# Optimization experiments

Measured on AMD Instinct MI355X. Metric: run time of the kernel, lower is better.

## Reference

```python
import jax, jax.numpy as jnp
import numpy as np

HIDDEN = 1024
NUM_CLASSES = 10
NUM_GAUSSIANS = 8
IN_FEATURES = 16
HEADS = NUM_CLASSES * NUM_GAUSSIANS * IN_FEATURES * 2  # 2560 tiny Linear(hidden,1) heads


def setup_inputs() -> dict:
    key = jax.random.key(0)
    kx, kw, kb = jax.random.split(key, 3)
    x = jax.random.normal(kx, (8192, HIDDEN), dtype=jnp.float32)
    # Stacked weights of the 2560 per-head Linear(hidden,1) layers.
    bound = 1.0 / np.sqrt(HIDDEN)
    W = jax.random.uniform(kw, (HIDDEN, HEADS), minval=-bound, maxval=bound, dtype=jnp.float32)
    b = jax.random.uniform(kb, (HEADS,), minval=-bound, maxval=bound, dtype=jnp.float32)
    return {"x": x, "W": W, "b": b}


def reference(x, W, b):
    batch = x.shape[0]
    # Fused form of the Python loop of Linear(hidden,1)+Sigmoid per head.
    z = jax.nn.sigmoid(x @ W + b)  # [batch, HEADS]
    return z.reshape(batch, NUM_CLASSES, NUM_GAUSSIANS, IN_FEATURES, 2)
```

## Files before the change

kernel.cpp:

```cpp
#include <hip/hip_runtime.h>
#include <hip/hip_bf16.h>

#define HIDDEN 1024
#define HEADS  2560

#define BM 256
#define BN 320
#define BK 64
#define NT (HIDDEN / BK)
#define AREG 0
#define ABYTES (BM * BK * 2)
#define BBYTES (BN * BK * 2)
#define BUFSZ  (ABYTES + BBYTES)

typedef float  f32x4  __attribute__((ext_vector_type(4)));
typedef __bf16 bf16x8 __attribute__((ext_vector_type(8)));
typedef __bf16 bf16x4 __attribute__((ext_vector_type(4)));

__device__ __forceinline__ void gload_lds16(const void* g, void* l) {
    __builtin_amdgcn_global_load_lds(
        (const __attribute__((address_space(1))) unsigned int*)g,
        (__attribute__((address_space(3))) unsigned int*)l, 16, 0, 0);
}
__device__ __forceinline__ unsigned swz(unsigned x) {
    return x ^ (((x >> 7) & 7u) << 4);
}

__global__ __launch_bounds__(256)
void cvt_x(const float* __restrict__ x, __bf16* __restrict__ xc, int n8)
{
    int idx = blockIdx.x * blockDim.x + threadIdx.x;
    int stride = gridDim.x * blockDim.x;
    for (int i = idx; i < n8; i += stride) {
        const float4 a = *reinterpret_cast<const float4*>(x + (size_t)i * 8);
        const float4 b = *reinterpret_cast<const float4*>(x + (size_t)i * 8 + 4);
        bf16x8 h;
        h[0] = (__bf16)a.x; h[1] = (__bf16)a.y; h[2] = (__bf16)a.z; h[3] = (__bf16)a.w;
        h[4] = (__bf16)b.x; h[5] = (__bf16)b.y; h[6] = (__bf16)b.z; h[7] = (__bf16)b.w;
        *reinterpret_cast<bf16x8*>(xc + (size_t)i * 8) = h;
    }
}

__global__ __launch_bounds__(256)
void cvt_w(const float* __restrict__ W, __bf16* __restrict__ Wt)
{
    __shared__ __bf16 tile[64][72];
    const int t  = threadIdx.x;
    const int n0 = blockIdx.x * 64;
    const int k0 = blockIdx.y * 64;

    #pragma unroll
    for (int i = 0; i < 4; ++i) {
        const int k    = (t >> 4) + i * 16;
        const int col4 = (t & 15) * 4;
        const float4 v = *reinterpret_cast<const float4*>(
            W + (size_t)(k0 + k) * HEADS + n0 + col4);
        bf16x4 h;
        h[0] = (__bf16)v.x; h[1] = (__bf16)v.y; h[2] = (__bf16)v.z; h[3] = (__bf16)v.w;
        *reinterpret_cast<bf16x4*>(&tile[k][col4]) = h;
    }
    __syncthreads();
    #pragma unroll
    for (int i = 0; i < 4; ++i) {
        const int n  = (t >> 4) + i * 16;
        const int k4 = (t & 15) * 4;
        bf16x4 h;
        h[0] = tile[k4 + 0][n]; h[1] = tile[k4 + 1][n];
        h[2] = tile[k4 + 2][n]; h[3] = tile[k4 + 3][n];
        *reinterpret_cast<bf16x4*>(Wt + (size_t)(n0 + n) * HIDDEN + k0 + k4) = h;
    }
}

__global__ __launch_bounds__(512, 2)
void gemm_p4(const __bf16* __restrict__ A, const __bf16* __restrict__ Bt,
             const float* __restrict__ bias, float* __restrict__ out)
{
    __shared__ char lds[2 * BUFSZ];

    const int t    = threadIdx.x;
    const int lane = t & 63;
    const int w    = t >> 6;
    const int wr   = w >> 2;
    const int wc   = w & 3;
    const int lhi  = lane >> 4;
    const int llo  = lane & 15;

    const int by  = blockIdx.x & 7;
    const int bx  = blockIdx.x >> 3;
    const int bm0 = bx * BM;
    const int bn0 = by * BN;

    const char* asrc[4]; unsigned adst[4];
    #pragma unroll
    for (int li = 0; li < 4; ++li) {
        unsigned d = (unsigned)(li * 8192 + t * 16);
        unsigned L = swz(d);
        asrc[li] = (const char*)A + (size_t)(bm0 + (L >> 7)) * (HIDDEN * 2) + (L & 127);
        adst[li] = d;
    }
    const char* bsrc[5]; unsigned bdst[5];
    #pragma unroll
    for (int li = 0; li < 5; ++li) {
        unsigned d = (unsigned)(li * 8192 + t * 16);
        unsigned L = swz(d);
        bsrc[li] = (const char*)Bt + (size_t)(bn0 + (L >> 7)) * (HIDDEN * 2) + (L & 127);
        bdst[li] = (unsigned)ABYTES + d;
    }

    const unsigned xa   = (unsigned)((llo & 7) << 4);
    const unsigned klo0 = ((unsigned)(lhi * 16)) ^ xa;
    const unsigned klo1 = ((unsigned)(64 + lhi * 16)) ^ xa;
    unsigned offA[8], offB[5];
    #pragma unroll
    for (int m = 0; m < 8; ++m)
        offA[m] = (unsigned)((wr * 128 + m * 16 + llo) * 128);
    #pragma unroll
    for (int n = 0; n < 5; ++n)
        offB[n] = (unsigned)ABYTES + (unsigned)((wc * 80 + n * 16 + llo) * 128);

    f32x4 acc[8][5];
    #pragma unroll
    for (int m = 0; m < 8; ++m)
        #pragma unroll
        for (int n = 0; n < 5; ++n)
            acc[m][n] = f32x4{0.f, 0.f, 0.f, 0.f};

    #pragma unroll
    for (int li = 0; li < 4; ++li) gload_lds16(asrc[li], lds + adst[li]);
    #pragma unroll
    for (int li = 0; li < 5; ++li) gload_lds16(bsrc[li], lds + bdst[li]);
    asm volatile("s_waitcnt vmcnt(0)" ::: "memory");
    __builtin_amdgcn_s_barrier();

    for (int k = 0; k < NT; ++k) {
        const char* buf = lds + (k & 1) * BUFSZ;
        char*       nbf = lds + ((k + 1) & 1) * BUFSZ;
        const bool  st  = (k + 1 < NT);
        const int   koff = (k + 1) * 128;

        bf16x8 af[4], bfr[5];

        #pragma unroll
        for (int m = 0; m < 4; ++m) af[m]  = *(const bf16x8*)(buf + (offA[m] + klo0));
        #pragma unroll
        for (int n = 0; n < 5; ++n) bfr[n] = *(const bf16x8*)(buf + (offB[n] + klo0));
        __builtin_amdgcn_s_barrier();
        asm volatile("s_waitcnt lgkmcnt(0)" ::: "memory");
        __builtin_amdgcn_sched_barrier(0);
        __builtin_amdgcn_s_setprio(1);
        #pragma unroll
        for (int m = 0; m < 4; ++m)
            #pragma unroll
            for (int n = 0; n < 5; ++n)
                acc[m][n] = __builtin_amdgcn_mfma_f32_16x16x32_bf16(
                    af[m], bfr[n], acc[m][n], 0, 0, 0);
        __builtin_amdgcn_s_setprio(0);
        if (st) {
            gload_lds16(asrc[0] + koff, nbf + adst[0]);
            gload_lds16(asrc[1] + koff, nbf + adst[1]);
            gload_lds16(asrc[2] + koff, nbf + adst[2]);
        }
        __builtin_amdgcn_s_barrier();

        #pragma unroll
        for (int m = 0; m < 4; ++m) af[m] = *(const bf16x8*)(buf + (offA[m + 4] + klo0));
        __builtin_amdgcn_s_barrier();
        asm volatile("s_waitcnt lgkmcnt(0)" ::: "memory");
        __builtin_amdgcn_sched_barrier(0);
        __builtin_amdgcn_s_setprio(1);
        #pragma unroll
        for (int m = 0; m < 4; ++m)
            #pragma unroll
            for (int n = 0; n < 5; ++n)
                acc[m + 4][n] = __builtin_amdgcn_mfma_f32_16x16x32_bf16(
                    af[m], bfr[n], acc[m + 4][n], 0, 0, 0);
        __builtin_amdgcn_s_setprio(0);
        if (st) {
            gload_lds16(asrc[3] + koff, nbf + adst[3]);
            gload_lds16(bsrc[0] + koff, nbf + bdst[0]);
            gload_lds16(bsrc[1] + koff, nbf + bdst[1]);
        }
        __builtin_amdgcn_s_barrier();

        #pragma unroll
        for (int m = 0; m < 4; ++m) af[m]  = *(const bf16x8*)(buf + (offA[m] + klo1));
        #pragma unroll
        for (int n = 0; n < 5; ++n) bfr[n] = *(const bf16x8*)(buf + (offB[n] + klo1));
        __builtin_amdgcn_s_barrier();
        asm volatile("s_waitcnt lgkmcnt(0)" ::: "memory");
        __builtin_amdgcn_sched_barrier(0);
        __builtin_amdgcn_s_setprio(1);
        #pragma unroll
        for (int m = 0; m < 4; ++m)
            #pragma unroll
            for (int n = 0; n < 5; ++n)
                acc[m][n] = __builtin_amdgcn_mfma_f32_16x16x32_bf16(
                    af[m], bfr[n], acc[m][n], 0, 0, 0);
        __builtin_amdgcn_s_setprio(0);
        if (st) {
            gload_lds16(bsrc[2] + koff, nbf + bdst[2]);
            gload_lds16(bsrc[3] + koff, nbf + bdst[3]);
            gload_lds16(bsrc[4] + koff, nbf + bdst[4]);
        }
        __builtin_amdgcn_s_barrier();

        #pragma unroll
        for (int m = 0; m < 4; ++m) af[m] = *(const bf16x8*)(buf + (offA[m + 4] + klo1));
        __builtin_amdgcn_s_barrier();
        asm volatile("s_waitcnt lgkmcnt(0)" ::: "memory");
        __builtin_amdgcn_sched_barrier(0);
        __builtin_amdgcn_s_setprio(1);
        #pragma unroll
        for (int m = 0; m < 4; ++m)
            #pragma unroll
            for (int n = 0; n < 5; ++n)
                acc[m + 4][n] = __builtin_amdgcn_mfma_f32_16x16x32_bf16(
                    af[m], bfr[n], acc[m + 4][n], 0, 0, 0);
        __builtin_amdgcn_s_setprio(0);
        asm volatile("s_waitcnt vmcnt(0)" ::: "memory");
        __builtin_amdgcn_s_barrier();
    }

    #pragma unroll
    for (int n = 0; n < 5; ++n) {
        const int col  = bn0 + wc * 80 + n * 16 + llo;
        const float bv = bias[col];
        #pragma unroll
        for (int m = 0; m < 8; ++m) {
            const int row0 = bm0 + wr * 128 + m * 16 + lhi * 4;
            #pragma unroll
            for (int r = 0; r < 4; ++r) {
                const float z = acc[m][n][r] + bv;
                out[(size_t)(row0 + r) * HEADS + col] = __fdividef(1.0f, 1.0f + __expf(-z));
            }
        }
    }
}

#define FBM 128
#define FBN 128
#define FBK 32
#define FLDK 40

__global__ __launch_bounds__(256)
void lch_gemm(const float* __restrict__ x, const float* __restrict__ W,
              const float* __restrict__ b, float* __restrict__ out)
{
    __shared__ __bf16 As[FBM][FLDK];
    __shared__ __bf16 Bs[FBN][FLDK];

    const int t   = threadIdx.x;
    const int bm0 = blockIdx.x * FBM;
    const int bn0 = blockIdx.y * FBN;
    const int lane = t & 63;
    const int wid  = t >> 6;
    const int wr   = wid >> 1;
    const int wc   = wid & 1;
    const int lhi  = lane >> 4;
    const int llo  = lane & 15;

    f32x4 acc[4][4];
    #pragma unroll
    for (int i = 0; i < 4; ++i)
        #pragma unroll
        for (int j = 0; j < 4; ++j)
            acc[i][j] = f32x4{0.f, 0.f, 0.f, 0.f};

    const int bn_col  = t & 127;
    const int bk_base = (t >> 7) * 16;

    for (int k0 = 0; k0 < HIDDEN; k0 += FBK) {
        #pragma unroll
        for (int i = 0; i < 4; ++i) {
            const int f   = t + i * 256;
            const int row = f >> 3;
            const int c4  = (f & 7) * 4;
            const float4 v = *reinterpret_cast<const float4*>(
                x + (size_t)(bm0 + row) * HIDDEN + k0 + c4);
            bf16x4 h;
            h[0] = (__bf16)v.x; h[1] = (__bf16)v.y;
            h[2] = (__bf16)v.z; h[3] = (__bf16)v.w;
            *reinterpret_cast<bf16x4*>(&As[row][c4]) = h;
        }
        {
            const float* wp = W + (size_t)(k0 + bk_base) * HEADS + bn0 + bn_col;
            bf16x8 h0, h1;
            #pragma unroll
            for (int i = 0; i < 8; ++i) h0[i] = (__bf16)wp[(size_t)i * HEADS];
            #pragma unroll
            for (int i = 0; i < 8; ++i) h1[i] = (__bf16)wp[(size_t)(i + 8) * HEADS];
            *reinterpret_cast<bf16x8*>(&Bs[bn_col][bk_base])     = h0;
            *reinterpret_cast<bf16x8*>(&Bs[bn_col][bk_base + 8]) = h1;
        }
        __syncthreads();

        bf16x8 af[4], bfr[4];
        #pragma unroll
        for (int i = 0; i < 4; ++i)
            af[i] = *reinterpret_cast<const bf16x8*>(&As[wr * 64 + i * 16 + llo][lhi * 8]);
        #pragma unroll
        for (int j = 0; j < 4; ++j)
            bfr[j] = *reinterpret_cast<const bf16x8*>(&Bs[wc * 64 + j * 16 + llo][lhi * 8]);
        #pragma unroll
        for (int i = 0; i < 4; ++i)
            #pragma unroll
            for (int j = 0; j < 4; ++j)
                acc[i][j] = __builtin_amdgcn_mfma_f32_16x16x32_bf16(
                    af[i], bfr[j], acc[i][j], 0, 0, 0);
        __syncthreads();
    }

    #pragma unroll
    for (int j = 0; j < 4; ++j) {
        const int col  = bn0 + wc * 64 + j * 16 + llo;
        const float bv = b[col];
        #pragma unroll
        for (int i = 0; i < 4; ++i) {
            const int row0 = bm0 + wr * 64 + i * 16 + lhi * 4;
            #pragma unroll
            for (int r = 0; r < 4; ++r) {
                const float z = acc[i][j][r] + bv;
                out[(size_t)(row0 + r) * HEADS + col] = 1.0f / (1.0f + __expf(-z));
            }
        }
    }
}

extern "C" void kernel_launch(void* const* d_in, const int* in_sizes, int n_in,
                              void* d_out, int out_size, void* d_ws, size_t ws_size,
                              hipStream_t stream) {
    const float* x = (const float*)d_in[0];
    const float* W = (const float*)d_in[1];
    const float* b = (const float*)d_in[2];
    float* out     = (float*)d_out;

    const int M = in_sizes[0] / HIDDEN;

    const size_t xc_bytes = (size_t)M * HIDDEN * sizeof(__bf16);
    const size_t wt_bytes = (size_t)HEADS * HIDDEN * sizeof(__bf16);

    if (ws_size >= xc_bytes + wt_bytes && (M % BM) == 0) {
        __bf16* xc = (__bf16*)d_ws;
        __bf16* Wt = (__bf16*)((char*)d_ws + xc_bytes);

        cvt_x<<<2048, 256, 0, stream>>>(x, xc, M * HIDDEN / 8);
        cvt_w<<<dim3(HEADS / 64, HIDDEN / 64), 256, 0, stream>>>(W, Wt);

        const int nwg = (M / BM) * (HEADS / BN);
        gemm_p4<<<nwg, 512, 0, stream>>>(xc, Wt, b, out);
    } else {
        dim3 grid(M / FBM, HEADS / FBN);
        lch_gemm<<<grid, dim3(256), 0, stream>>>(x, W, b, out);
    }
}
```

Measured before the change: 68.98 us.

## Replace four-phase ping-pong GEMM loop with simple double-buffered prefetch

The main loop no longer interleaves MFMA quarters with partial global-to-LDS loads, intra-iteration barriers and priority switches. It issues every prefetch for the next K tile at the top of the iteration, then runs two half-K MFMA passes over the full 8x5 fragment set with one barrier per iteration. Per-load source and destination arrays collapse into a single base pointer plus constant strides to save registers. This drops barrier and scheduling overhead but gives up the fine-grained overlap, and holding 8 A fragments at once raises register pressure under the 2-waves-per-SIMD bound.

Result: faster. 67.01 us (-2.8%).

```diff
diff --git a/kernel.cpp b/kernel.cpp
--- a/kernel.cpp
+++ b/kernel.cpp
@@ -8,7 +8,6 @@
 #define BN 320
 #define BK 64
 #define NT (HIDDEN / BK)
-#define AREG 0
 #define ABYTES (BM * BK * 2)
 #define BBYTES (BN * BK * 2)
 #define BUFSZ  (ABYTES + BBYTES)
@@ -72,7 +71,7 @@
 }
 
 __global__ __launch_bounds__(512, 2)
-void gemm_p4(const __bf16* __restrict__ A, const __bf16* __restrict__ Bt,
+void gemm_dl(const __bf16* __restrict__ A, const __bf16* __restrict__ Bt,
              const float* __restrict__ bias, float* __restrict__ out)
 {
     __shared__ char lds[2 * BUFSZ];
@@ -90,22 +89,12 @@
     const int bm0 = bx * BM;
     const int bn0 = by * BN;
 
-    const char* asrc[4]; unsigned adst[4];
-    #pragma unroll
-    for (int li = 0; li < 4; ++li) {
-        unsigned d = (unsigned)(li * 8192 + t * 16);
-        unsigned L = swz(d);
-        asrc[li] = (const char*)A + (size_t)(bm0 + (L >> 7)) * (HIDDEN * 2) + (L & 127);
-        adst[li] = d;
-    }
-    const char* bsrc[5]; unsigned bdst[5];
-    #pragma unroll
-    for (int li = 0; li < 5; ++li) {
-        unsigned d = (unsigned)(li * 8192 + t * 16);
-        unsigned L = swz(d);
-        bsrc[li] = (const char*)Bt + (size_t)(bn0 + (L >> 7)) * (HIDDEN * 2) + (L & 127);
-        bdst[li] = (unsigned)ABYTES + d;
-    }
+    const unsigned d0 = (unsigned)(t * 16);
+    const unsigned L0 = swz(d0);
+    const char* asrc0 = (const char*)A  + (size_t)(bm0 + (L0 >> 7)) * (HIDDEN * 2) + (L0 & 127);
+    const char* bsrc0 = (const char*)Bt + (size_t)(bn0 + (L0 >> 7)) * (HIDDEN * 2) + (L0 & 127);
+    char* adst0 = (char*)lds + d0;
+    char* bdst0 = (char*)lds + ABYTES + d0;
 
     const unsigned xa   = (unsigned)((llo & 7) << 4);
     const unsigned klo0 = ((unsigned)(lhi * 16)) ^ xa;
@@ -126,97 +115,53 @@
             acc[m][n] = f32x4{0.f, 0.f, 0.f, 0.f};
 
     #pragma unroll
-    for (int li = 0; li < 4; ++li) gload_lds16(asrc[li], lds + adst[li]);
-    #pragma unroll
-    for (int li = 0; li < 5; ++li) gload_lds16(bsrc[li], lds + bdst[li]);
+    for (int li = 0; li < 4; ++li) gload_lds16(asrc0 + li * 131072, adst0 + li * 8192);
+    #pragma unroll
+    for (int li = 0; li < 5; ++li) gload_lds16(bsrc0 + li * 131072, bdst0 + li * 8192);
     asm volatile("s_waitcnt vmcnt(0)" ::: "memory");
     __builtin_amdgcn_s_barrier();
 
     for (int k = 0; k < NT; ++k) {
-        const char* buf = lds + (k & 1) * BUFSZ;
-        char*       nbf = lds + ((k + 1) & 1) * BUFSZ;
-        const bool  st  = (k + 1 < NT);
+        const char* buf  = lds + (k & 1) * BUFSZ;
+        const unsigned nb = (unsigned)(((k + 1) & 1) * BUFSZ);
         const int   koff = (k + 1) * 128;
 
-        bf16x8 af[4], bfr[5];
-
-        #pragma unroll
-        for (int m = 0; m < 4; ++m) af[m]  = *(const bf16x8*)(buf + (offA[m] + klo0));
-        #pragma unroll
-        for (int n = 0; n < 5; ++n) bfr[n] = *(const bf16x8*)(buf + (offB[n] + klo0));
-        __builtin_amdgcn_s_barrier();
-        asm volatile("s_waitcnt lgkmcnt(0)" ::: "memory");
-        __builtin_amdgcn_sched_barrier(0);
-        __builtin_amdgcn_s_setprio(1);
-        #pragma unroll
-        for (int m = 0; m < 4; ++m)
-            #pragma unroll
-            for (int n = 0; n < 5; ++n)
-                acc[m][n] = __builtin_amdgcn_mfma_f32_16x16x32_bf16(
-                    af[m], bfr[n], acc[m][n], 0, 0, 0);
-        __builtin_amdgcn_s_setprio(0);
-        if (st) {
-            gload_lds16(asrc[0] + koff, nbf + adst[0]);
-            gload_lds16(asrc[1] + koff, nbf + adst[1]);
-            gload_lds16(asrc[2] + koff, nbf + adst[2]);
-        }
-        __builtin_amdgcn_s_barrier();
-
-        #pragma unroll
-        for (int m = 0; m < 4; ++m) af[m] = *(const bf16x8*)(buf + (offA[m + 4] + klo0));
-        __builtin_amdgcn_s_barrier();
-        asm volatile("s_waitcnt lgkmcnt(0)" ::: "memory");
-        __builtin_amdgcn_sched_barrier(0);
-        __builtin_amdgcn_s_setprio(1);
-        #pragma unroll
-        for (int m = 0; m < 4; ++m)
-            #pragma unroll
-            for (int n = 0; n < 5; ++n)
-                acc[m + 4][n] = __builtin_amdgcn_mfma_f32_16x16x32_bf16(
-                    af[m], bfr[n], acc[m + 4][n], 0, 0, 0);
-        __builtin_amdgcn_s_setprio(0);
-        if (st) {
-            gload_lds16(asrc[3] + koff, nbf + adst[3]);
-            gload_lds16(bsrc[0] + koff, nbf + bdst[0]);
-            gload_lds16(bsrc[1] + koff, nbf + bdst[1]);
-        }
-        __builtin_amdgcn_s_barrier();
-
-        #pragma unroll
-        for (int m = 0; m < 4; ++m) af[m]  = *(const bf16x8*)(buf + (offA[m] + klo1));
-        #pragma unroll
-        for (int n = 0; n < 5; ++n) bfr[n] = *(const bf16x8*)(buf + (offB[n] + klo1));
-        __builtin_amdgcn_s_barrier();
-        asm volatile("s_waitcnt lgkmcnt(0)" ::: "memory");
-        __builtin_amdgcn_sched_barrier(0);
-        __builtin_amdgcn_s_setprio(1);
-        #pragma unroll
-        for (int m = 0; m < 4; ++m)
-            #pragma unroll
-            for (int n = 0; n < 5; ++n)
-                acc[m][n] = __builtin_amdgcn_mfma_f32_16x16x32_bf16(
-                    af[m], bfr[n], acc[m][n], 0, 0, 0);
-        __builtin_amdgcn_s_setprio(0);
-        if (st) {
-            gload_lds16(bsrc[2] + koff, nbf + bdst[2]);
-            gload_lds16(bsrc[3] + koff, nbf + bdst[3]);
-            gload_lds16(bsrc[4] + koff, nbf + bdst[4]);
-        }
-        __builtin_amdgcn_s_barrier();
-
-        #pragma unroll
-        for (int m = 0; m < 4; ++m) af[m] = *(const bf16x8*)(buf + (offA[m + 4] + klo1));
-        __builtin_amdgcn_s_barrier();
-        asm volatile("s_waitcnt lgkmcnt(0)" ::: "memory");
-        __builtin_amdgcn_sched_barrier(0);
-        __builtin_amdgcn_s_setprio(1);
-        #pragma unroll
-        for (int m = 0; m < 4; ++m)
-            #pragma unroll
-            for (int n = 0; n < 5; ++n)
-                acc[m + 4][n] = __builtin_amdgcn_mfma_f32_16x16x32_bf16(
-                    af[m], bfr[n], acc[m + 4][n], 0, 0, 0);
-        __builtin_amdgcn_s_setprio(0);
+        if (k + 1 < NT) {
+            #pragma unroll
+            for (int li = 0; li < 4; ++li)
+                gload_lds16(asrc0 + li * 131072 + koff, adst0 + nb + li * 8192);
+            #pragma unroll
+            for (int li = 0; li < 5; ++li)
+                gload_lds16(bsrc0 + li * 131072 + koff, bdst0 + nb + li * 8192);
+        }
+
+        {
+            bf16x8 af[8], bfr[5];
+            #pragma unroll
+            for (int m = 0; m < 8; ++m) af[m]  = *(const bf16x8*)(buf + (offA[m] + klo0));
+            #pragma unroll
+            for (int n = 0; n < 5; ++n) bfr[n] = *(const bf16x8*)(buf + (offB[n] + klo0));
+            #pragma unroll
+            for (int m = 0; m < 8; ++m)
+                #pragma unroll
+                for (int n = 0; n < 5; ++n)
+                    acc[m][n] = __builtin_amdgcn_mfma_f32_16x16x32_bf16(
+                        af[m], bfr[n], acc[m][n], 0, 0, 0);
+        }
+        {
+            bf16x8 af[8], bfr[5];
+            #pragma unroll
+            for (int m = 0; m < 8; ++m) af[m]  = *(const bf16x8*)(buf + (offA[m] + klo1));
+            #pragma unroll
+            for (int n = 0; n < 5; ++n) bfr[n] = *(const bf16x8*)(buf + (offB[n] + klo1));
+            #pragma unroll
+            for (int m = 0; m < 8; ++m)
+                #pragma unroll
+                for (int n = 0; n < 5; ++n)
+                    acc[m][n] = __builtin_amdgcn_mfma_f32_16x16x32_bf16(
+                        af[m], bfr[n], acc[m][n], 0, 0, 0);
+        }
+
         asm volatile("s_waitcnt vmcnt(0)" ::: "memory");
         __builtin_amdgcn_s_barrier();
     }
@@ -347,7 +292,7 @@
         cvt_w<<<dim3(HEADS / 64, HIDDEN / 64), 256, 0, stream>>>(W, Wt);
 
         const int nwg = (M / BM) * (HEADS / BN);
-        gemm_p4<<<nwg, 512, 0, stream>>>(xc, Wt, b, out);
+        gemm_dl<<<nwg, 512, 0, stream>>>(xc, Wt, b, out);
     } else {
         dim3 grid(M / FBM, HEADS / FBN);
         lch_gemm<<<grid, dim3(256), 0, stream>>>(x, W, b, out);
```
